# Kernel tuning notes

Measured on AMD Instinct MI355X. Metric: run time of the kernel, lower is better.

## Reference

```python
import jax, jax.numpy as jnp
import numpy as np

B, N, D, H, HID = 8, 512, 512, 8, 2048


def setup_inputs() -> dict:
    key = jax.random.key(0)
    ks = jax.random.split(key, 8)
    s = 0.02
    p = lambda i, shape: jax.random.normal(ks[i], shape, jnp.float32) * s
    return dict(
        x=jax.random.normal(ks[0], (B, N, D), jnp.float32),
        Wq=p(1, (D, D)), bq=jnp.zeros((D,), jnp.float32),
        Wk=p(2, (D, D)), bk=jnp.zeros((D,), jnp.float32),
        Wv=p(3, (D, D)), bv=jnp.zeros((D,), jnp.float32),
        Wsig=p(4, (H, D)), bsig=jnp.zeros((H,), jnp.float32),
        ln1_g=jnp.ones((D,), jnp.float32), ln1_b=jnp.zeros((D,), jnp.float32),
        W1=p(5, (HID, D)), b1=jnp.zeros((HID,), jnp.float32),
        W2=p(6, (D, HID)), b2=jnp.zeros((D,), jnp.float32),
        ln2_g=jnp.ones((D,), jnp.float32), ln2_b=jnp.zeros((D,), jnp.float32),
    )


def _ln(z, g, b, eps=1e-5):
    m = jnp.mean(z, axis=-1, keepdims=True)
    v = jnp.var(z, axis=-1, keepdims=True)
    return (z - m) * jax.lax.rsqrt(v + eps) * g + b


def reference(x, Wq, bq, Wk, bk, Wv, bv, Wsig, bsig,
              ln1_g, ln1_b, W1, b1, W2, b2, ln2_g, ln2_b):
    Bb, Nn, Dd = x.shape
    Hh = bsig.shape[0]
    dh = Dd // Hh
    # --- AnomalyAttention: series attention S, Gaussian prior P, Z = S @ V ---
    Q = (x @ Wq.T + bq).reshape(Bb, Nn, Hh, dh)
    K = (x @ Wk.T + bk).reshape(Bb, Nn, Hh, dh)
    V = (x @ Wv.T + bv).reshape(Bb, Nn, Hh, dh)
    scores = jnp.einsum('bnhd,bmhd->bhnm', Q, K) / jnp.sqrt(jnp.float32(dh))
    S = jax.nn.softmax(scores, axis=-1)                       # [B,H,N,N]
    # learned positive scale sigma per (batch, position, head)
    sigma = jax.nn.softplus(x @ Wsig.T + bsig) + 1e-5         # [B,N,H]
    idx = jnp.arange(Nn, dtype=jnp.float32)
    dist2 = (idx[:, None] - idx[None, :]) ** 2                # [N,N]
    sig = jnp.transpose(sigma, (0, 2, 1))[..., None]          # [B,H,N,1]
    gauss = jnp.exp(-dist2 / (2.0 * sig * sig)) / (jnp.sqrt(2.0 * jnp.pi) * sig)
    P = gauss / jnp.sum(gauss, axis=-1, keepdims=True)        # row-normalized prior
    Zh = jnp.einsum('bhnm,bmhd->bnhd', S, V).reshape(Bb, Nn, Dd)
    # --- residual + LayerNorm + MLP(relu) + residual + LayerNorm ---
    Z = _ln(Zh + x, ln1_g, ln1_b)
    hidden = jax.nn.relu(Z @ W1.T + b1)
    x_hat = hidden @ W2.T + b2
    x_hat = _ln(x_hat + Z, ln2_g, ln2_b)
    return (x_hat, P, S)
```

## Files before the change

### kernel.cpp

```cpp
#include <hip/hip_runtime.h>
#include <cstdint>

typedef short s16x8 __attribute__((ext_vector_type(8)));
typedef float f32x4 __attribute__((ext_vector_type(4)));
using u16 = unsigned short;


__device__ __forceinline__ u16 f2bf(float f) {
    union { float f; uint32_t u; } v; v.f = f;
    uint32_t u = v.u;
    return (u16)((u + 0x7FFFu + ((u >> 16) & 1u)) >> 16);
}

__device__ __forceinline__ s16x8 pack_bf8(f32x4 a, f32x4 b) {
    union { s16x8 s; uint32_t w[4]; } o;
    uint32_t a0 = __float_as_uint(a[0]), a1 = __float_as_uint(a[1]);
    uint32_t a2 = __float_as_uint(a[2]), a3 = __float_as_uint(a[3]);
    uint32_t b0 = __float_as_uint(b[0]), b1 = __float_as_uint(b[1]);
    uint32_t b2 = __float_as_uint(b[2]), b3 = __float_as_uint(b[3]);
    o.w[0] = (a0 >> 16) | (a1 & 0xffff0000u);
    o.w[1] = (a2 >> 16) | (a3 & 0xffff0000u);
    o.w[2] = (b0 >> 16) | (b1 & 0xffff0000u);
    o.w[3] = (b2 >> 16) | (b3 & 0xffff0000u);
    return o.s;
}

__global__ __launch_bounds__(256) void k_convert(
    const float* __restrict__ x, const float* __restrict__ wq,
    const float* __restrict__ wk, const float* __restrict__ wv,
    const float* __restrict__ w1, const float* __restrict__ w2,
    const float* __restrict__ bq, const float* __restrict__ bk,
    const float* __restrict__ bv,
    u16* __restrict__ xb, u16* __restrict__ wqb, u16* __restrict__ wkb,
    u16* __restrict__ wvb, u16* __restrict__ w1b, u16* __restrict__ w2b,
    float* __restrict__ biascat)
{
    long g = (long)blockIdx.x * 256 + threadIdx.x;
    if (g >= 1245184) {
        long id = g - 1245184;
        if (id < 384) {
            const float* src = id < 128 ? bq : id < 256 ? bk : bv;
            ((float4*)biascat)[id] = ((const float4*)src)[id & 127];
        }
        return;
    }
    const float* src; u16* dst; long off;
    if      (g <  524288) { src = x;  dst = xb;  off = g; }
    else if (g <  589824) { src = wq; dst = wqb; off = g -  524288; }
    else if (g <  655360) { src = wk; dst = wkb; off = g -  589824; }
    else if (g <  720896) { src = wv; dst = wvb; off = g -  655360; }
    else if (g <  983040) { src = w1; dst = w1b; off = g -  720896; }
    else                  { src = w2; dst = w2b; off = g -  983040; }
    float4 v = ((const float4*)src)[off];
    ushort4 o;
    o.x = f2bf(v.x); o.y = f2bf(v.y); o.z = f2bf(v.z); o.w = f2bf(v.w);
    ((ushort4*)dst)[off] = o;
}

__global__ __launch_bounds__(256) void k_sigma(
    const float* __restrict__ x, const float* __restrict__ Wsig,
    const float* __restrict__ bsig, float* __restrict__ sigT)
{
    int row  = (int)((blockIdx.x * 256 + threadIdx.x) >> 6);
    int lane = threadIdx.x & 63;
    const float4* xr = (const float4*)(x + (long)row * 512);
    float4 xa = xr[lane * 2], xc = xr[lane * 2 + 1];
    float xs[8] = {xa.x, xa.y, xa.z, xa.w, xc.x, xc.y, xc.z, xc.w};
    float ph[8];
#pragma unroll
    for (int h = 0; h < 8; ++h) {
        const float4* wr = (const float4*)(Wsig + h * 512);
        float4 wa = wr[lane * 2], wc = wr[lane * 2 + 1];
        ph[h] = xs[0]*wa.x + xs[1]*wa.y + xs[2]*wa.z + xs[3]*wa.w
              + xs[4]*wc.x + xs[5]*wc.y + xs[6]*wc.z + xs[7]*wc.w;
    }
#pragma unroll
    for (int h = 0; h < 8; ++h)
#pragma unroll
        for (int m = 1; m < 64; m <<= 1)
            ph[h] += __shfl_xor(ph[h], m, 64);
    if (lane < 8) {
        float z  = ph[lane] + bsig[lane];
        float sp = fmaxf(z, 0.f) + log1pf(__expf(-fabsf(z)));
        int b = row >> 9, n = row & 511;
        sigT[(((long)b * 8 + lane) << 9) + n] = sp + 1e-5f;
    }
}

__global__ __launch_bounds__(256) void k_prior(
    const float* __restrict__ sigT, float* __restrict__ P)
{
    int row  = (int)((blockIdx.x * 256 + threadIdx.x) >> 6);
    int lane = threadIdx.x & 63;
    int n = row & 511;
    float s = sigT[row];
    float a = -1.0f / (2.0f * s * s);
    float e[8]; float sum = 0.f;
#pragma unroll
    for (int j = 0; j < 8; ++j) {
        float d = (float)(n - (lane * 8 + j));
        e[j] = __expf(a * d * d);
        sum += e[j];
    }
#pragma unroll
    for (int m = 1; m < 64; m <<= 1) sum += __shfl_xor(sum, m, 64);
    float r = 1.0f / sum;
    float4* dst = (float4*)(P + (long)row * 512 + lane * 8);
    dst[0] = make_float4(e[0]*r, e[1]*r, e[2]*r, e[3]*r);
    dst[1] = make_float4(e[4]*r, e[5]*r, e[6]*r, e[7]*r);
}

template<int BM, int BN, int BK, int WM, int WN, int EPI, typename TA>
__global__ __launch_bounds__(256) void k_gemm_nt(
    const TA* __restrict__ A, const u16* __restrict__ B,
    const float* __restrict__ bias, void* __restrict__ C,
    int lda, int ldb, int K, long sA, long sB)
{
    constexpr int LDP = BK + 8;
    __shared__ u16 As[BM][LDP];
    __shared__ u16 Bs[BN][LDP];

    const TA*  Ag = A + (long)blockIdx.z * sA + (long)blockIdx.x * BM * lda;
    const u16* Bg = B + (long)blockIdx.z * sB + (long)blockIdx.y * BN * ldb;

    int tid  = threadIdx.x;
    int wave = tid >> 6, lane = tid & 63;
    int wm = wave / WN, wn = wave % WN;
    constexpr int WTM = BM / WM, WTN = BN / WN;
    constexpr int FM = WTM / 16, FN = WTN / 16;

    f32x4 acc[FM][FN];
#pragma unroll
    for (int i = 0; i < FM; ++i)
#pragma unroll
        for (int j = 0; j < FN; ++j) acc[i][j] = (f32x4){0.f, 0.f, 0.f, 0.f};

    for (int k0 = 0; k0 < K; k0 += BK) {
        __syncthreads();
        constexpr int ACH = BM * BK / 8 / 256;
#pragma unroll
        for (int c = 0; c < ACH; ++c) {
            int id = c * 256 + tid;
            int r = id / (BK / 8), c8 = id % (BK / 8);
            *(s16x8*)&As[r][c8 * 8] = *(const s16x8*)(Ag + (long)r * lda + k0 + c8 * 8);
        }
        constexpr int BCH = BN * BK / 8 / 256;
#pragma unroll
        for (int c = 0; c < BCH; ++c) {
            int id = c * 256 + tid;
            int r = id / (BK / 8), c8 = id % (BK / 8);
            *(s16x8*)&Bs[r][c8 * 8] = *(const s16x8*)(Bg + (long)r * ldb + k0 + c8 * 8);
        }
        __syncthreads();
#pragma unroll
        for (int kk = 0; kk < BK / 32; ++kk) {
            s16x8 af[FM], bfr[FN];
#pragma unroll
            for (int fm = 0; fm < FM; ++fm)
                af[fm] = *(const s16x8*)&As[wm * WTM + fm * 16 + (lane & 15)][kk * 32 + (lane >> 4) * 8];
#pragma unroll
            for (int fn = 0; fn < FN; ++fn)
                bfr[fn] = *(const s16x8*)&Bs[wn * WTN + fn * 16 + (lane & 15)][kk * 32 + (lane >> 4) * 8];
#pragma unroll
            for (int fm = 0; fm < FM; ++fm)
#pragma unroll
                for (int fn = 0; fn < FN; ++fn)
                    acc[fm][fn] = __builtin_amdgcn_mfma_f32_16x16x32_bf16(af[fm], bfr[fn], acc[fm][fn], 0, 0, 0);
        }
    }

    int i0 = blockIdx.x * BM + wm * WTM;
    int j0 = blockIdx.y * BN + wn * WTN;
#pragma unroll
    for (int fm = 0; fm < FM; ++fm)
#pragma unroll
        for (int fn = 0; fn < FN; ++fn)
#pragma unroll
            for (int j = 0; j < 4; ++j) {
                int gi = i0 + fm * 16 + ((lane >> 4) << 2) + j;
                int gj = j0 + fn * 16 + (lane & 15);
                float v = acc[fm][fn][j];
                if constexpr (EPI == 3) {
                    v = fmaxf(v + bias[gj], 0.f);
                    ((u16*)C)[(long)gi * 2048 + gj] = f2bf(v);
                } else if constexpr (EPI == 4) {
                    ((float*)C)[(long)gi * 512 + gj] = v + bias[gj];
                } else {
                    v += bias[gj];
                    int mat = gj >> 9, cj = gj & 511;
                    int h = cj >> 6, d = cj & 63, b = gi >> 9, n = gi & 511;
                    u16* base = (u16*)C;
                    if (mat == 0)
                        base[(((long)(b * 8 + h) * 512 + n) << 6) + d] = f2bf(v);
                    else if (mat == 1)
                        (base + 2097152)[(((long)(b * 8 + h) * 512 + n) << 6) + d] = f2bf(v);
                    else
                        (base + 4194304)[(((long)(b * 8 + h) * 64 + d) << 9) + n] = f2bf(v);
                }
            }
}

__global__ __launch_bounds__(256) void k_attn_pv(
    const u16* __restrict__ Qb, const u16* __restrict__ Kb,
    const u16* __restrict__ Vt, float* __restrict__ S, float* __restrict__ Zh)
{
    __shared__ float Sb[4][16][260];
    int bh = blockIdx.y;
    int rb = blockIdx.x;
    int tid = threadIdx.x;
    int wave = tid >> 6, lane = tid & 63;
    int r16 = lane & 15, g4 = lane >> 4, hi8 = g4 * 8;

    const u16* Qg = Qb + ((long)bh * 512 + rb * 64 + wave * 16) * 64;
    const u16* Kg = Kb + (long)bh * 512 * 64;
    const u16* Vg = Vt + (long)bh * 64 * 512;

    s16x8 qa[2];
    qa[0] = *(const s16x8*)(Qg + r16 * 64 + hi8);
    qa[1] = *(const s16x8*)(Qg + r16 * 64 + 32 + hi8);

    f32x4 acc[32];
#pragma unroll
    for (int t = 0; t < 32; ++t) acc[t] = (f32x4){0.f, 0.f, 0.f, 0.f};

#pragma unroll
    for (int ch = 0; ch < 4; ++ch)
#pragma unroll
        for (int kk = 0; kk < 2; ++kk)
#pragma unroll
            for (int fn = 0; fn < 8; ++fn) {
                s16x8 b = *(const s16x8*)(Kg + (long)(ch * 128 + fn * 16 + r16) * 64 + kk * 32 + hi8);
                acc[ch * 8 + fn] = __builtin_amdgcn_mfma_f32_16x16x32_bf16(qa[kk], b, acc[ch * 8 + fn], 0, 0, 0);
            }

    float mx[4] = {-1e30f, -1e30f, -1e30f, -1e30f};
#pragma unroll
    for (int t = 0; t < 32; ++t)
#pragma unroll
        for (int j = 0; j < 4; ++j) mx[j] = fmaxf(mx[j], acc[t][j]);
#pragma unroll
    for (int j = 0; j < 4; ++j)
#pragma unroll
        for (int m = 1; m < 16; m <<= 1) mx[j] = fmaxf(mx[j], __shfl_xor(mx[j], m, 64));

    float sum[4] = {0.f, 0.f, 0.f, 0.f};
#pragma unroll
    for (int t = 0; t < 32; ++t)
#pragma unroll
        for (int j = 0; j < 4; ++j) {
            float p = __expf(0.125f * (acc[t][j] - mx[j]));
            acc[t][j] = p;
            sum[j] += p;
        }
#pragma unroll
    for (int j = 0; j < 4; ++j) {
#pragma unroll
        for (int m = 1; m < 16; m <<= 1) sum[j] += __shfl_xor(sum[j], m, 64);
        sum[j] = 1.0f / sum[j];
    }
#pragma unroll
    for (int t = 0; t < 32; ++t)
#pragma unroll
        for (int j = 0; j < 4; ++j) acc[t][j] *= sum[j];

    long sbase = ((long)bh * 512 + rb * 64 + wave * 16) * 512;
#pragma unroll
    for (int t = 0; t < 32; ++t) {
        int col = t * 16 + r16;
#pragma unroll
        for (int j = 0; j < 4; ++j)
            S[sbase + (long)(g4 * 4 + j) * 512 + col] = acc[t][j];
    }

    f32x4 zacc[4];
#pragma unroll
    for (int fn = 0; fn < 4; ++fn) zacc[fn] = (f32x4){0.f, 0.f, 0.f, 0.f};

#pragma unroll
    for (int p = 0; p < 2; ++p) {
#pragma unroll
        for (int t = 0; t < 16; ++t)
#pragma unroll
            for (int j = 0; j < 4; ++j)
                Sb[wave][g4 * 4 + j][t * 16 + r16] = acc[p * 16 + t][j];
#pragma unroll
        for (int kk = 0; kk < 8; ++kk) {
            f32x4 lo = *(const f32x4*)&Sb[wave][r16][kk * 32 + hi8];
            f32x4 hi = *(const f32x4*)&Sb[wave][r16][kk * 32 + hi8 + 4];
            s16x8 pa = pack_bf8(lo, hi);
#pragma unroll
            for (int fn = 0; fn < 4; ++fn) {
                s16x8 vb = *(const s16x8*)(Vg + (long)(fn * 16 + r16) * 512 + p * 256 + kk * 32 + hi8);
                zacc[fn] = __builtin_amdgcn_mfma_f32_16x16x32_bf16(pa, vb, zacc[fn], 0, 0, 0);
            }
        }
    }

    long zb = ((long)(bh >> 3) * 512 + rb * 64 + wave * 16) * 512 + (bh & 7) * 64;
#pragma unroll
    for (int fn = 0; fn < 4; ++fn)
#pragma unroll
        for (int j = 0; j < 4; ++j)
            Zh[zb + (long)(g4 * 4 + j) * 512 + fn * 16 + r16] = zacc[fn][j];
}

template<bool WBF>
__global__ __launch_bounds__(256) void k_ln(
    const float* __restrict__ a, const float* __restrict__ b,
    const float* __restrict__ g, const float* __restrict__ bt,
    float* __restrict__ y, u16* __restrict__ yb)
{
    int row  = (int)((blockIdx.x * 256 + threadIdx.x) >> 6);
    int lane = threadIdx.x & 63;
    const float4* ar = (const float4*)(a + (long)row * 512);
    const float4* br = (const float4*)(b + (long)row * 512);
    float4 a0 = ar[lane * 2], a1 = ar[lane * 2 + 1];
    float4 b0 = br[lane * 2], b1 = br[lane * 2 + 1];
    float v[8] = {a0.x + b0.x, a0.y + b0.y, a0.z + b0.z, a0.w + b0.w,
                  a1.x + b1.x, a1.y + b1.y, a1.z + b1.z, a1.w + b1.w};
    float s = 0.f, q = 0.f;
#pragma unroll
    for (int j = 0; j < 8; ++j) { s += v[j]; q += v[j] * v[j]; }
#pragma unroll
    for (int m = 1; m < 64; m <<= 1) {
        s += __shfl_xor(s, m, 64);
        q += __shfl_xor(q, m, 64);
    }
    float mean = s * (1.f / 512.f);
    float var  = q * (1.f / 512.f) - mean * mean;
    float rstd = rsqrtf(var + 1e-5f);
    const float4* gr = (const float4*)(g + lane * 8);
    const float4* tr = (const float4*)(bt + lane * 8);
    float4 g0 = gr[0], g1 = gr[1], t0 = tr[0], t1 = tr[1];
    float gg[8] = {g0.x, g0.y, g0.z, g0.w, g1.x, g1.y, g1.z, g1.w};
    float tt[8] = {t0.x, t0.y, t0.z, t0.w, t1.x, t1.y, t1.z, t1.w};
    float o[8];
#pragma unroll
    for (int j = 0; j < 8; ++j) o[j] = (v[j] - mean) * rstd * gg[j] + tt[j];
    float4* yr = (float4*)(y + (long)row * 512 + lane * 8);
    yr[0] = make_float4(o[0], o[1], o[2], o[3]);
    yr[1] = make_float4(o[4], o[5], o[6], o[7]);
    if constexpr (WBF) {
        s16x8 ob;
#pragma unroll
        for (int j = 0; j < 8; ++j) ob[j] = (short)f2bf(o[j]);
        *(s16x8*)(yb + (long)row * 512 + lane * 8) = ob;
    }
}

extern "C" void kernel_launch(void* const* d_in, const int* in_sizes, int n_in,
                              void* d_out, int out_size, void* d_ws, size_t ws_size,
                              hipStream_t stream)
{
    const float* x    = (const float*)d_in[0];
    const float* Wq   = (const float*)d_in[1];
    const float* bq   = (const float*)d_in[2];
    const float* Wk   = (const float*)d_in[3];
    const float* bk   = (const float*)d_in[4];
    const float* Wv   = (const float*)d_in[5];
    const float* bv   = (const float*)d_in[6];
    const float* Wsig = (const float*)d_in[7];
    const float* bsig = (const float*)d_in[8];
    const float* g1   = (const float*)d_in[9];
    const float* be1  = (const float*)d_in[10];
    const float* W1   = (const float*)d_in[11];
    const float* b1   = (const float*)d_in[12];
    const float* W2   = (const float*)d_in[13];
    const float* b2   = (const float*)d_in[14];
    const float* g2   = (const float*)d_in[15];
    const float* be2  = (const float*)d_in[16];

    float* out_xhat = (float*)d_out;
    float* out_P    = out_xhat + 2097152;
    float* out_S    = out_P + 16777216;

    char* ws = (char*)d_ws;
    u16*   xb   = (u16*)(ws + 0);
    u16*   Qb   = (u16*)(ws + 4194304);
    u16*   hid  = (u16*)(ws + 0);
    u16*   Wqb  = (u16*)(ws + 16777216);
    u16*   Wkb  = (u16*)(ws + 17301504);
    u16*   Wvb  = (u16*)(ws + 17825792);
    u16*   W1b  = (u16*)(ws + 18350080);
    u16*   W2b  = (u16*)(ws + 20447232);
    float* sigT = (float*)(ws + 22544384);
    float* Zh   = (float*)(ws + 22675456);
    float* bcat = (float*)(ws + 22675456);
    float* x2   = (float*)(ws + 22675456);
    float* Z    = (float*)(ws + 31064064);
    u16*   Zb   = (u16*)(ws + 39452672);

    k_convert<<<4866, 256, 0, stream>>>(x, Wq, Wk, Wv, W1, W2, bq, bk, bv,
                                        xb, Wqb, Wkb, Wvb, W1b, W2b, bcat);
    k_sigma<<<1024, 256, 0, stream>>>(x, Wsig, bsig, sigT);
    k_prior<<<8192, 256, 0, stream>>>(sigT, out_P);

    k_gemm_nt<128,128,64,2,2,5,u16><<<dim3(32,12,1),256,0,stream>>>(
        xb, Wqb, bcat, Qb, 512, 512, 512, 0, 0);

    k_attn_pv<<<dim3(8,64),256,0,stream>>>(Qb, Qb + 2097152, Qb + 4194304, out_S, Zh);

    k_ln<true><<<1024,256,0,stream>>>(Zh, x, g1, be1, Z, Zb);

    k_gemm_nt<128,128,64,2,2,3,u16><<<dim3(32,16,1),256,0,stream>>>(Zb, W1b, b1, hid, 512, 512, 512, 0, 0);

    k_gemm_nt<128,64,64,2,2,4,u16><<<dim3(32,8,1),256,0,stream>>>(hid, W2b, b2, x2, 2048, 2048, 2048, 0, 0);

    k_ln<false><<<1024,256,0,stream>>>(x2, Z, g2, be2, out_xhat, nullptr);
}
```

Baseline: 154.4 us.

## Use direct global-to-LDS loads in GEMMs, fuse sigma into convert, retile W2 GEMM

The GEMM kernel now stages tiles with global_load_lds, loading straight into LDS without passing through registers. The shared tiles become unpadded 64-wide rows, which may add LDS bank conflicts on fragment reads. The sigma projection is folded into the convert kernel as extra blocks, removing one launch. The W2 GEMM now uses 64x64 tiles with more blocks.

```diff
diff --git a/kernel.cpp b/kernel.cpp
--- a/kernel.cpp
+++ b/kernel.cpp
@@ -10,6 +10,12 @@
     union { float f; uint32_t u; } v; v.f = f;
     uint32_t u = v.u;
     return (u16)((u + 0x7FFFu + ((u >> 16) & 1u)) >> 16);
+}
+
+__device__ __forceinline__ void gload_lds16(const void* g, void* l) {
+    __builtin_amdgcn_global_load_lds(
+        (const __attribute__((address_space(1))) unsigned int*)g,
+        (__attribute__((address_space(3))) unsigned int*)l, 16, 0, 0);
 }
 
 __device__ __forceinline__ s16x8 pack_bf8(f32x4 a, f32x4 b) {
@@ -25,17 +31,47 @@
     return o.s;
 }
 
-__global__ __launch_bounds__(256) void k_convert(
+__global__ __launch_bounds__(256) void k_convert_sigma(
     const float* __restrict__ x, const float* __restrict__ wq,
     const float* __restrict__ wk, const float* __restrict__ wv,
     const float* __restrict__ w1, const float* __restrict__ w2,
     const float* __restrict__ bq, const float* __restrict__ bk,
     const float* __restrict__ bv,
+    const float* __restrict__ Wsig, const float* __restrict__ bsig,
     u16* __restrict__ xb, u16* __restrict__ wqb, u16* __restrict__ wkb,
     u16* __restrict__ wvb, u16* __restrict__ w1b, u16* __restrict__ w2b,
-    float* __restrict__ biascat)
-{
-    long g = (long)blockIdx.x * 256 + threadIdx.x;
+    float* __restrict__ biascat, float* __restrict__ sigT)
+{
+    int bk_ = blockIdx.x;
+    int tid = threadIdx.x;
+    if (bk_ >= 4866) {
+        int row  = (int)(((bk_ - 4866) * 256 + tid) >> 6);
+        int lane = tid & 63;
+        const float4* xr = (const float4*)(x + (long)row * 512);
+        float4 xa = xr[lane * 2], xc = xr[lane * 2 + 1];
+        float xs[8] = {xa.x, xa.y, xa.z, xa.w, xc.x, xc.y, xc.z, xc.w};
+        float ph[8];
+#pragma unroll
+        for (int h = 0; h < 8; ++h) {
+            const float4* wr = (const float4*)(Wsig + h * 512);
+            float4 wa = wr[lane * 2], wc = wr[lane * 2 + 1];
+            ph[h] = xs[0]*wa.x + xs[1]*wa.y + xs[2]*wa.z + xs[3]*wa.w
+                  + xs[4]*wc.x + xs[5]*wc.y + xs[6]*wc.z + xs[7]*wc.w;
+        }
+#pragma unroll
+        for (int h = 0; h < 8; ++h)
+#pragma unroll
+            for (int m = 1; m < 64; m <<= 1)
+                ph[h] += __shfl_xor(ph[h], m, 64);
+        if (lane < 8) {
+            float z  = ph[lane] + bsig[lane];
+            float sp = fmaxf(z, 0.f) + log1pf(__expf(-fabsf(z)));
+            int b = row >> 9, n = row & 511;
+            sigT[(((long)b * 8 + lane) << 9) + n] = sp + 1e-5f;
+        }
+        return;
+    }
+    long g = (long)bk_ * 256 + tid;
     if (g >= 1245184) {
         long id = g - 1245184;
         if (id < 384) {
@@ -57,36 +93,6 @@
     ((ushort4*)dst)[off] = o;
 }
 
-__global__ __launch_bounds__(256) void k_sigma(
-    const float* __restrict__ x, const float* __restrict__ Wsig,
-    const float* __restrict__ bsig, float* __restrict__ sigT)
-{
-    int row  = (int)((blockIdx.x * 256 + threadIdx.x) >> 6);
-    int lane = threadIdx.x & 63;
-    const float4* xr = (const float4*)(x + (long)row * 512);
-    float4 xa = xr[lane * 2], xc = xr[lane * 2 + 1];
-    float xs[8] = {xa.x, xa.y, xa.z, xa.w, xc.x, xc.y, xc.z, xc.w};
-    float ph[8];
-#pragma unroll
-    for (int h = 0; h < 8; ++h) {
-        const float4* wr = (const float4*)(Wsig + h * 512);
-        float4 wa = wr[lane * 2], wc = wr[lane * 2 + 1];
-        ph[h] = xs[0]*wa.x + xs[1]*wa.y + xs[2]*wa.z + xs[3]*wa.w
-              + xs[4]*wc.x + xs[5]*wc.y + xs[6]*wc.z + xs[7]*wc.w;
-    }
-#pragma unroll
-    for (int h = 0; h < 8; ++h)
-#pragma unroll
-        for (int m = 1; m < 64; m <<= 1)
-            ph[h] += __shfl_xor(ph[h], m, 64);
-    if (lane < 8) {
-        float z  = ph[lane] + bsig[lane];
-        float sp = fmaxf(z, 0.f) + log1pf(__expf(-fabsf(z)));
-        int b = row >> 9, n = row & 511;
-        sigT[(((long)b * 8 + lane) << 9) + n] = sp + 1e-5f;
-    }
-}
-
 __global__ __launch_bounds__(256) void k_prior(
     const float* __restrict__ sigT, float* __restrict__ P)
 {
@@ -110,57 +116,59 @@
     dst[1] = make_float4(e[4]*r, e[5]*r, e[6]*r, e[7]*r);
 }
 
-template<int BM, int BN, int BK, int WM, int WN, int EPI, typename TA>
+template<int BM, int BN, int EPI>
 __global__ __launch_bounds__(256) void k_gemm_nt(
-    const TA* __restrict__ A, const u16* __restrict__ B,
+    const u16* __restrict__ A, const u16* __restrict__ B,
     const float* __restrict__ bias, void* __restrict__ C,
-    int lda, int ldb, int K, long sA, long sB)
-{
-    constexpr int LDP = BK + 8;
-    __shared__ u16 As[BM][LDP];
-    __shared__ u16 Bs[BN][LDP];
-
-    const TA*  Ag = A + (long)blockIdx.z * sA + (long)blockIdx.x * BM * lda;
-    const u16* Bg = B + (long)blockIdx.z * sB + (long)blockIdx.y * BN * ldb;
+    int lda, int ldb, int K)
+{
+    constexpr int BK = 64;
+    __shared__ __align__(16) u16 As[BM * BK];
+    __shared__ __align__(16) u16 Bs[BN * BK];
+
+    const u16* Ag = A + (long)blockIdx.x * BM * lda;
+    const u16* Bg = B + (long)blockIdx.y * BN * ldb;
 
     int tid  = threadIdx.x;
     int wave = tid >> 6, lane = tid & 63;
-    int wm = wave / WN, wn = wave % WN;
-    constexpr int WTM = BM / WM, WTN = BN / WN;
+    int wm = wave >> 1, wn = wave & 1;
+    constexpr int WTM = BM / 2, WTN = BN / 2;
     constexpr int FM = WTM / 16, FN = WTN / 16;
+    int r16 = lane & 15, hi8 = (lane >> 4) * 8;
 
     f32x4 acc[FM][FN];
 #pragma unroll
     for (int i = 0; i < FM; ++i)
 #pragma unroll
         for (int j = 0; j < FN; ++j) acc[i][j] = (f32x4){0.f, 0.f, 0.f, 0.f};
+
+    constexpr int nA = BM * BK / 2048;
+    constexpr int nB = BN * BK / 2048;
 
     for (int k0 = 0; k0 < K; k0 += BK) {
         __syncthreads();
-        constexpr int ACH = BM * BK / 8 / 256;
-#pragma unroll
-        for (int c = 0; c < ACH; ++c) {
-            int id = c * 256 + tid;
-            int r = id / (BK / 8), c8 = id % (BK / 8);
-            *(s16x8*)&As[r][c8 * 8] = *(const s16x8*)(Ag + (long)r * lda + k0 + c8 * 8);
-        }
-        constexpr int BCH = BN * BK / 8 / 256;
-#pragma unroll
-        for (int c = 0; c < BCH; ++c) {
-            int id = c * 256 + tid;
-            int r = id / (BK / 8), c8 = id % (BK / 8);
-            *(s16x8*)&Bs[r][c8 * 8] = *(const s16x8*)(Bg + (long)r * ldb + k0 + c8 * 8);
+#pragma unroll
+        for (int c = 0; c < nA; ++c) {
+            int e = (c * 256 + tid) * 8;
+            int r = e >> 6, col = e & 63;
+            gload_lds16(Ag + (long)r * lda + k0 + col, &As[e]);
+        }
+#pragma unroll
+        for (int c = 0; c < nB; ++c) {
+            int e = (c * 256 + tid) * 8;
+            int r = e >> 6, col = e & 63;
+            gload_lds16(Bg + (long)r * ldb + k0 + col, &Bs[e]);
         }
         __syncthreads();
 #pragma unroll
-        for (int kk = 0; kk < BK / 32; ++kk) {
+        for (int kk = 0; kk < 2; ++kk) {
             s16x8 af[FM], bfr[FN];
 #pragma unroll
             for (int fm = 0; fm < FM; ++fm)
-                af[fm] = *(const s16x8*)&As[wm * WTM + fm * 16 + (lane & 15)][kk * 32 + (lane >> 4) * 8];
+                af[fm] = *(const s16x8*)&As[(wm * WTM + fm * 16 + r16) * 64 + kk * 32 + hi8];
 #pragma unroll
             for (int fn = 0; fn < FN; ++fn)
-                bfr[fn] = *(const s16x8*)&Bs[wn * WTN + fn * 16 + (lane & 15)][kk * 32 + (lane >> 4) * 8];
+                bfr[fn] = *(const s16x8*)&Bs[(wn * WTN + fn * 16 + r16) * 64 + kk * 32 + hi8];
 #pragma unroll
             for (int fm = 0; fm < FM; ++fm)
 #pragma unroll
@@ -178,7 +186,7 @@
 #pragma unroll
             for (int j = 0; j < 4; ++j) {
                 int gi = i0 + fm * 16 + ((lane >> 4) << 2) + j;
-                int gj = j0 + fn * 16 + (lane & 15);
+                int gj = j0 + fn * 16 + r16;
                 float v = acc[fm][fn][j];
                 if constexpr (EPI == 3) {
                     v = fmaxf(v + bias[gj], 0.f);
@@ -379,8 +387,6 @@
     u16*   Qb   = (u16*)(ws + 4194304);
     u16*   hid  = (u16*)(ws + 0);
     u16*   Wqb  = (u16*)(ws + 16777216);
-    u16*   Wkb  = (u16*)(ws + 17301504);
-    u16*   Wvb  = (u16*)(ws + 17825792);
     u16*   W1b  = (u16*)(ws + 18350080);
     u16*   W2b  = (u16*)(ws + 20447232);
     float* sigT = (float*)(ws + 22544384);
@@ -390,21 +396,25 @@
     float* Z    = (float*)(ws + 31064064);
     u16*   Zb   = (u16*)(ws + 39452672);
 
-    k_convert<<<4866, 256, 0, stream>>>(x, Wq, Wk, Wv, W1, W2, bq, bk, bv,
-                                        xb, Wqb, Wkb, Wvb, W1b, W2b, bcat);
-    k_sigma<<<1024, 256, 0, stream>>>(x, Wsig, bsig, sigT);
+    u16* Wkb = Wqb + 262144;
+    u16* Wvb = Wqb + 524288;
+
+    k_convert_sigma<<<5890, 256, 0, stream>>>(x, Wq, Wk, Wv, W1, W2, bq, bk, bv,
+                                              Wsig, bsig,
+                                              xb, Wqb, Wkb, Wvb, W1b, W2b,
+                                              bcat, sigT);
     k_prior<<<8192, 256, 0, stream>>>(sigT, out_P);
 
-    k_gemm_nt<128,128,64,2,2,5,u16><<<dim3(32,12,1),256,0,stream>>>(
-        xb, Wqb, bcat, Qb, 512, 512, 512, 0, 0);
+    k_gemm_nt<128,128,5><<<dim3(32,12,1),256,0,stream>>>(
+        xb, Wqb, bcat, Qb, 512, 512, 512);
 
     k_attn_pv<<<dim3(8,64),256,0,stream>>>(Qb, Qb + 2097152, Qb + 4194304, out_S, Zh);
 
     k_ln<true><<<1024,256,0,stream>>>(Zh, x, g1, be1, Z, Zb);
 
-    k_gemm_nt<128,128,64,2,2,3,u16><<<dim3(32,16,1),256,0,stream>>>(Zb, W1b, b1, hid, 512, 512, 512, 0, 0);
-
-    k_gemm_nt<128,64,64,2,2,4,u16><<<dim3(32,8,1),256,0,stream>>>(hid, W2b, b2, x2, 2048, 2048, 2048, 0, 0);
+    k_gemm_nt<128,128,3><<<dim3(32,16,1),256,0,stream>>>(Zb, W1b, b1, hid, 512, 512, 512);
+
+    k_gemm_nt<64,64,4><<<dim3(64,8,1),256,0,stream>>>(hid, W2b, b2, x2, 2048, 2048, 2048);
 
     k_ln<false><<<1024,256,0,stream>>>(x2, Z, g2, be2, out_xhat, nullptr);
 }
```

Measured after the change: 155.5 us. No clear change (+0.7%).
